# Performance work log

Measured on AMD Instinct MI355X. Metric: run time of the kernel, lower is better.

Reference implementation:

```python
import jax, jax.numpy as jnp
import numpy as np

N, E, F_IN, HID, N_LAYERS, C_OUT = 100000, 1600000, 256, 64, 5, 64


def _glorot(k, shape):
    lim = np.sqrt(6.0 / (shape[0] + shape[1])).astype(np.float32)
    return jax.random.uniform(k, shape, jnp.float32, -lim, lim)


def setup_inputs() -> dict:
    key = jax.random.key(0)
    ks = jax.random.split(key, 16)
    inp = {
        'feats': jax.random.normal(ks[0], (N, F_IN), jnp.float32),
        'src': jax.random.randint(ks[1], (E,), 0, N),
        'dst': jax.random.randint(ks[2], (E,), 0, N),
    }
    dims = [F_IN] + [HID] * N_LAYERS
    for i in range(N_LAYERS):
        inp[f'W{i}'] = _glorot(ks[3 + i], (dims[i], dims[i + 1]))
        inp[f'b{i}'] = jnp.zeros((dims[i + 1],), jnp.float32)
    inp['Wout'] = _glorot(ks[10], (HID * N_LAYERS, C_OUT))
    inp['bout'] = jnp.zeros((C_OUT,), jnp.float32)
    return inp


def reference(feats, src, dst, W0, b0, W1, b1, W2, b2, W3, b3, W4, b4, Wout, bout):
    n = feats.shape[0]
    one = jnp.ones((src.shape[0],), feats.dtype)
    out_deg = jnp.zeros((n,), feats.dtype).at[src].add(one)
    in_deg = jnp.zeros((n,), feats.dtype).at[dst].add(one)
    # DGL GraphConv norm='both': D_out^{-1/2} on src side, D_in^{-1/2} on dst side
    norm_src = jax.lax.rsqrt(jnp.maximum(out_deg, 1.0))
    norm_dst = jax.lax.rsqrt(jnp.maximum(in_deg, 1.0))

    h = feats
    feat_lst = []
    for W, b in [(W0, b0), (W1, b1), (W2, b2), (W3, b3), (W4, b4)]:
        hs = (h * norm_src[:, None]) @ W          # weight before gather (in>=out)
        agg = jax.ops.segment_sum(hs[src], dst, num_segments=n)  # [N, hid]
        h = jax.nn.relu(agg * norm_dst[:, None] + b)
        feat_lst.append(h)                        # dropout is identity in eval

    out = jnp.concatenate(feat_lst, axis=-1)      # JK 'cat': [N, 5*hid]
    # update_all(copy_u, sum): unnormalized neighbor sum
    hfin = jax.ops.segment_sum(out[src], dst, num_segments=n)
    return hfin @ Wout + bout
```

## Files before the change

kernel.cpp:

```cpp
#include <hip/hip_runtime.h>

#define FIN 256
#define HID 64
#define NLAYERS 5

#define FMA4(ACC, S, V) { float _s = (S); ACC.x += _s*(V).x; ACC.y += _s*(V).y; ACC.z += _s*(V).z; ACC.w += _s*(V).w; }

__device__ inline unsigned short f2bf(float f) {
  unsigned u = __float_as_uint(f);
  u += 0x7FFF + ((u >> 16) & 1);
  return (unsigned short)(u >> 16);
}
__device__ inline float bf2f(unsigned short s) { return __uint_as_float(((unsigned)s) << 16); }

__global__ __launch_bounds__(256) void k_count(const int* __restrict__ dst,
                                               int* __restrict__ cd, int* __restrict__ rank,
                                               int E, int half) {
  int i = blockIdx.x * 256 + threadIdx.x;
  if (i < half) rank[i] = atomicAdd(&cd[dst[i]], 1);
  int i2 = i + half;
  if (i2 < E) rank[i2] = atomicAdd(&cd[dst[i2]], 1);
}

__global__ __launch_bounds__(256) void k_rowalloc(const int* __restrict__ cnt, int* __restrict__ row_start,
                                                  int* __restrict__ gcur, int n) {
  int i = blockIdx.x * 256 + threadIdx.x;
  int lane = threadIdx.x & 63;
  int c = (i < n) ? cnt[i] : 0;
  int s = c;
  #pragma unroll
  for (int d = 1; d < 64; d <<= 1) {
    int t = __shfl_up(s, d, 64);
    if (lane >= d) s += t;
  }
  int total = __shfl(s, 63, 64);
  int base = 0;
  if (lane == 63) base = atomicAdd(gcur, total);
  base = __shfl(base, 63, 64);
  int start = base + s - c;
  if (i < n) row_start[i] = start;
}

__global__ __launch_bounds__(256) void k_place(const int* __restrict__ src, const int* __restrict__ dst,
                                               const int* __restrict__ rank, const int* __restrict__ row_start,
                                               int* __restrict__ col, int* __restrict__ cs, int E) {
  int e = blockIdx.x * 256 + threadIdx.x;
  if (e < E) {
    int s = src[e];
    col[row_start[dst[e]] + rank[e]] = s;
    atomicAdd(&cs[s], 1);
  }
}

__global__ __launch_bounds__(256) void k_norm(const int* __restrict__ cnt, float* __restrict__ nrm, int n) {
  int i = blockIdx.x * 256 + threadIdx.x;
  if (i < n) nrm[i] = rsqrtf(fmaxf((float)cnt[i], 1.0f));
}

#define G0PAD 36
__global__ __launch_bounds__(256) void k_gemm0(const float* __restrict__ feats, const float* __restrict__ ns,
                                               const float* __restrict__ W0, unsigned short* __restrict__ hs,
                                               int nrows) {
  __shared__ float sA[64 * G0PAD];
  __shared__ float sW[32 * 64];
  const int tid = threadIdx.x;
  const int row0 = blockIdx.x * 64;
  const int tr4 = (tid >> 4) * 4;
  const int tc4 = (tid & 15) * 4;
  const int sr = tid >> 3;
  const int sc = (tid & 7) * 4;
  const int wk = tid >> 3;
  float4 acc0 = {0,0,0,0}, acc1 = {0,0,0,0}, acc2 = {0,0,0,0}, acc3 = {0,0,0,0};
  const float4 z4 = {0,0,0,0};

  for (int kb = 0; kb < FIN; kb += 32) {
    __syncthreads();
    {
      int r1 = row0 + sr, r2 = row0 + sr + 32;
      float4 v1 = (r1 < nrows) ? *(const float4*)&feats[(size_t)r1 * FIN + kb + sc] : z4;
      float4 v2 = (r2 < nrows) ? *(const float4*)&feats[(size_t)r2 * FIN + kb + sc] : z4;
      *(float4*)&sA[sr * G0PAD + sc] = v1;
      *(float4*)&sA[(sr + 32) * G0PAD + sc] = v2;
      *(float4*)&sW[wk * 64 + sc]      = *(const float4*)&W0[(size_t)(kb + wk) * HID + sc];
      *(float4*)&sW[wk * 64 + sc + 32] = *(const float4*)&W0[(size_t)(kb + wk) * HID + sc + 32];
    }
    __syncthreads();
    #pragma unroll
    for (int kc = 0; kc < 32; kc += 4) {
      float4 a0 = *(const float4*)&sA[(tr4 + 0) * G0PAD + kc];
      float4 a1 = *(const float4*)&sA[(tr4 + 1) * G0PAD + kc];
      float4 a2 = *(const float4*)&sA[(tr4 + 2) * G0PAD + kc];
      float4 a3 = *(const float4*)&sA[(tr4 + 3) * G0PAD + kc];
      #define G0STEP(KK, C) { \
        float4 wv = *(const float4*)&sW[(kc + KK) * 64 + tc4]; \
        FMA4(acc0, a0.C, wv); FMA4(acc1, a1.C, wv); FMA4(acc2, a2.C, wv); FMA4(acc3, a3.C, wv); }
      G0STEP(0, x) G0STEP(1, y) G0STEP(2, z) G0STEP(3, w)
      #undef G0STEP
    }
  }
  #pragma unroll
  for (int r = 0; r < 4; ++r) {
    int row = row0 + tr4 + r;
    if (row < nrows) {
      float s = ns[row];
      float4 o = (r == 0) ? acc0 : (r == 1) ? acc1 : (r == 2) ? acc2 : acc3;
      ushort4 p;
      p.x = f2bf(o.x * s); p.y = f2bf(o.y * s); p.z = f2bf(o.z * s); p.w = f2bf(o.w * s);
      *(ushort4*)&hs[(size_t)row * HID + tc4] = p;
    }
  }
}

#define GDPAD 68
template<bool HASW, bool FIRST>
__global__ __launch_bounds__(256, 4) void k_gemm_dual(const unsigned short* __restrict__ h,
                                                      const float* __restrict__ ns,
                                                      const float* __restrict__ W, const float* __restrict__ Wb,
                                                      unsigned short* __restrict__ hs, float* __restrict__ proj,
                                                      int nrows) {
  __shared__ float sA[64 * GDPAD];
  __shared__ float sW[64 * 64];
  __shared__ float sWb[64 * 64];
  const int tid = threadIdx.x;
  const int row0 = blockIdx.x * 64;
  const int tr4 = (tid >> 4) * 4;
  const int tc4 = (tid & 15) * 4;
  const int sr = tid >> 2;
  const int scb = (tid & 3) * 16;
  const float4 z4 = {0,0,0,0};

  {
    int gr = row0 + sr;
    #pragma unroll
    for (int o = 0; o < 16; o += 4) {
      float4 v = z4;
      if (gr < nrows) {
        ushort4 u = *(const ushort4*)&h[(size_t)gr * HID + scb + o];
        v.x = bf2f(u.x); v.y = bf2f(u.y); v.z = bf2f(u.z); v.w = bf2f(u.w);
      }
      *(float4*)&sA[sr * GDPAD + scb + o] = v;
      if (HASW) *(float4*)&sW[sr * 64 + scb + o] = *(const float4*)&W[(size_t)sr * HID + scb + o];
      *(float4*)&sWb[sr * 64 + scb + o] = *(const float4*)&Wb[(size_t)sr * HID + scb + o];
    }
  }
  __syncthreads();

  float4 aw0 = {0,0,0,0}, aw1 = {0,0,0,0}, aw2 = {0,0,0,0}, aw3 = {0,0,0,0};
  float4 ab0 = {0,0,0,0}, ab1 = {0,0,0,0}, ab2 = {0,0,0,0}, ab3 = {0,0,0,0};
  #pragma unroll 2
  for (int kc = 0; kc < 64; kc += 4) {
    float4 a0 = *(const float4*)&sA[(tr4 + 0) * GDPAD + kc];
    float4 a1 = *(const float4*)&sA[(tr4 + 1) * GDPAD + kc];
    float4 a2 = *(const float4*)&sA[(tr4 + 2) * GDPAD + kc];
    float4 a3 = *(const float4*)&sA[(tr4 + 3) * GDPAD + kc];
    #define GDSTEP(KK, C) { \
      if (HASW) { \
        float4 wv = *(const float4*)&sW[(kc + KK) * 64 + tc4]; \
        FMA4(aw0, a0.C, wv); FMA4(aw1, a1.C, wv); FMA4(aw2, a2.C, wv); FMA4(aw3, a3.C, wv); } \
      { float4 wbv = *(const float4*)&sWb[(kc + KK) * 64 + tc4]; \
        FMA4(ab0, a0.C, wbv); FMA4(ab1, a1.C, wbv); FMA4(ab2, a2.C, wbv); FMA4(ab3, a3.C, wbv); } }
    GDSTEP(0, x) GDSTEP(1, y) GDSTEP(2, z) GDSTEP(3, w)
    #undef GDSTEP
  }

  #pragma unroll
  for (int r = 0; r < 4; ++r) {
    int row = row0 + tr4 + r;
    if (row < nrows) {
      float4 ob = (r == 0) ? ab0 : (r == 1) ? ab1 : (r == 2) ? ab2 : ab3;
      float4 p;
      if (FIRST) {
        p = ob;
      } else {
        p = *(const float4*)&proj[(size_t)row * HID + tc4];
        p.x += ob.x; p.y += ob.y; p.z += ob.z; p.w += ob.w;
      }
      if (HASW) {
        float s = ns[row];
        float4 o = (r == 0) ? aw0 : (r == 1) ? aw1 : (r == 2) ? aw2 : aw3;
        ushort4 pk;
        pk.x = f2bf(o.x * s); pk.y = f2bf(o.y * s); pk.z = f2bf(o.z * s); pk.w = f2bf(o.w * s);
        *(ushort4*)&hs[(size_t)row * HID + tc4] = pk;
        *(float4*)&proj[(size_t)row * HID + tc4] = p;
      } else {
        ushort4 pk;
        pk.x = f2bf(p.x); pk.y = f2bf(p.y); pk.z = f2bf(p.z); pk.w = f2bf(p.w);
        *(ushort4*)&hs[(size_t)row * HID + tc4] = pk;
      }
    }
  }
}

template<bool FINAL>
__global__ __launch_bounds__(256) void k_gather_bf(const int* __restrict__ row_start, const int* __restrict__ cnt,
                                                   const int* __restrict__ col, const unsigned short* __restrict__ x,
                                                   const float* __restrict__ nd, const float* __restrict__ b,
                                                   unsigned short* __restrict__ ybf, float* __restrict__ yf,
                                                   int n) {
  int node = blockIdx.x * 4 + (threadIdx.x >> 6);
  if (node >= n) return;
  int lane = threadIdx.x & 63;
  int g = lane >> 4;
  int fl = (lane & 15) * 4;
  int j0 = row_start[node];
  int jend = j0 + cnt[node];
  float4 acc = {0,0,0,0}, acc2 = {0,0,0,0};
  int j = j0 + g;
  for (; j + 4 < jend; j += 8) {
    int s1 = col[j];
    int s2 = col[j + 4];
    ushort4 u1 = *(const ushort4*)&x[(size_t)s1 * HID + fl];
    ushort4 u2 = *(const ushort4*)&x[(size_t)s2 * HID + fl];
    acc.x  += bf2f(u1.x); acc.y  += bf2f(u1.y); acc.z  += bf2f(u1.z); acc.w  += bf2f(u1.w);
    acc2.x += bf2f(u2.x); acc2.y += bf2f(u2.y); acc2.z += bf2f(u2.z); acc2.w += bf2f(u2.w);
  }
  if (j < jend) {
    int s = col[j];
    ushort4 u = *(const ushort4*)&x[(size_t)s * HID + fl];
    acc.x += bf2f(u.x); acc.y += bf2f(u.y); acc.z += bf2f(u.z); acc.w += bf2f(u.w);
  }
  acc.x += acc2.x; acc.y += acc2.y; acc.z += acc2.z; acc.w += acc2.w;
  #pragma unroll
  for (int m = 16; m <= 32; m <<= 1) {
    acc.x += __shfl_xor(acc.x, m, 64);
    acc.y += __shfl_xor(acc.y, m, 64);
    acc.z += __shfl_xor(acc.z, m, 64);
    acc.w += __shfl_xor(acc.w, m, 64);
  }
  if (g == 0) {
    float4 bb = *(const float4*)&b[fl];
    if (FINAL) {
      float4 o = {acc.x + bb.x, acc.y + bb.y, acc.z + bb.z, acc.w + bb.w};
      *(float4*)&yf[(size_t)node * HID + fl] = o;
    } else {
      float s = nd[node];
      ushort4 pk;
      pk.x = f2bf(fmaxf(acc.x * s + bb.x, 0.f));
      pk.y = f2bf(fmaxf(acc.y * s + bb.y, 0.f));
      pk.z = f2bf(fmaxf(acc.z * s + bb.z, 0.f));
      pk.w = f2bf(fmaxf(acc.w * s + bb.w, 0.f));
      *(ushort4*)&ybf[(size_t)node * HID + fl] = pk;
    }
  }
}

extern "C" void kernel_launch(void* const* d_in, const int* in_sizes, int n_in,
                              void* d_out, int out_size, void* d_ws, size_t ws_size,
                              hipStream_t stream) {
  const float* feats = (const float*)d_in[0];
  const int* src = (const int*)d_in[1];
  const int* dst = (const int*)d_in[2];
  const float* W[NLAYERS]    = {(const float*)d_in[3], (const float*)d_in[5], (const float*)d_in[7],
                                (const float*)d_in[9], (const float*)d_in[11]};
  const float* bias[NLAYERS] = {(const float*)d_in[4], (const float*)d_in[6], (const float*)d_in[8],
                                (const float*)d_in[10], (const float*)d_in[12]};
  const float* Wout = (const float*)d_in[13];
  const float* bout = (const float*)d_in[14];
  float* out = (float*)d_out;

  const int N = in_sizes[0] / FIN;
  const int E = in_sizes[1];
  const size_t Np = (size_t)((N + 63) / 64) * 64;
  const size_t Ep = (size_t)((E + 63) / 64) * 64;

  char* w = (char*)d_ws;
  int* cnt_s     = (int*)w;            w += Np * 4;
  int* cnt_d     = (int*)w;            w += Np * 4;
  int* row_start = (int*)w;            w += Np * 4;
  int* gcur      = (int*)w;            w += 64 * 4;
  int* col       = (int*)w;            w += Ep * 4;
  float* norm_s  = (float*)w;          w += Np * 4;
  float* norm_d  = (float*)w;          w += Np * 4;
  unsigned short* h = (unsigned short*)w;      w += Np * HID * 2;
  float* proj    = (float*)w;          w += Np * HID * 4;
  unsigned short* hsbuf = (unsigned short*)w;  w += Np * HID * 2;
  int* rank = (int*)h;

  (void)hipMemsetAsync(cnt_s, 0, 2 * Np * sizeof(int), stream);
  (void)hipMemsetAsync(gcur, 0, sizeof(int), stream);

  const int half = (E + 1) / 2;
  k_count<<<(half + 255) / 256, 256, 0, stream>>>(dst, cnt_d, rank, E, half);
  k_rowalloc<<<(N + 255) / 256, 256, 0, stream>>>(cnt_d, row_start, gcur, N);
  k_place<<<(E + 255) / 256, 256, 0, stream>>>(src, dst, rank, row_start, col, cnt_s, E);
  k_norm<<<(int)((2 * Np + 255) / 256), 256, 0, stream>>>(cnt_s, norm_s, (int)(2 * Np));

  const int GEMMB = (N + 63) / 64;
  k_gemm0<<<GEMMB, 256, 0, stream>>>(feats, norm_s, W[0], hsbuf, N);

  const int GB = (N + 3) / 4;
  for (int i = 0; i < NLAYERS; ++i) {
    k_gather_bf<false><<<GB, 256, 0, stream>>>(row_start, cnt_d, col, hsbuf, norm_d, bias[i], h, nullptr, N);
    const float* Wb = Wout + (size_t)i * HID * HID;
    if (i == 0) {
      k_gemm_dual<true, true><<<GEMMB, 256, 0, stream>>>(h, norm_s, W[1], Wb, hsbuf, proj, N);
    } else if (i < NLAYERS - 1) {
      k_gemm_dual<true, false><<<GEMMB, 256, 0, stream>>>(h, norm_s, W[i + 1], Wb, hsbuf, proj, N);
    } else {
      k_gemm_dual<false, false><<<GEMMB, 256, 0, stream>>>(h, norm_s, nullptr, Wb, hsbuf, proj, N);
    }
  }
  k_gather_bf<true><<<GB, 256, 0, stream>>>(row_start, cnt_d, col, hsbuf, nullptr, bout, nullptr, out, N);
}
```

Measured before the change: 638.9 us.

## Keep per-layer bf16 activations and compute JK projection in one final kernel

Replaces the dual GEMM, which accumulated the Wout projection into an fp32 proj buffer every layer (a read and a write per layer), with single-weight GEMMs. Each layer's bf16 activations are now stored in their own buffer, and one k_jk kernel computes the concatenated projection at the end. The gather loop is also unrolled to four independent loads per iteration for more memory-level parallelism. In exchange the workspace is larger and the final kernel reads all five activation buffers.

```diff
diff --git a/kernel.cpp b/kernel.cpp
--- a/kernel.cpp
+++ b/kernel.cpp
@@ -112,81 +112,118 @@
 }
 
 #define GDPAD 68
-template<bool HASW, bool FIRST>
-__global__ __launch_bounds__(256, 4) void k_gemm_dual(const unsigned short* __restrict__ h,
-                                                      const float* __restrict__ ns,
-                                                      const float* __restrict__ W, const float* __restrict__ Wb,
-                                                      unsigned short* __restrict__ hs, float* __restrict__ proj,
-                                                      int nrows) {
+__global__ __launch_bounds__(256, 4) void k_gemm_single(const unsigned short* __restrict__ h,
+                                                        const float* __restrict__ ns,
+                                                        const float* __restrict__ W,
+                                                        unsigned short* __restrict__ hs, int nrows) {
   __shared__ float sA[64 * GDPAD];
   __shared__ float sW[64 * 64];
-  __shared__ float sWb[64 * 64];
   const int tid = threadIdx.x;
   const int row0 = blockIdx.x * 64;
   const int tr4 = (tid >> 4) * 4;
   const int tc4 = (tid & 15) * 4;
   const int sr = tid >> 2;
   const int scb = (tid & 3) * 16;
-  const float4 z4 = {0,0,0,0};
 
   {
     int gr = row0 + sr;
     #pragma unroll
     for (int o = 0; o < 16; o += 4) {
-      float4 v = z4;
+      float4 v = {0,0,0,0};
       if (gr < nrows) {
         ushort4 u = *(const ushort4*)&h[(size_t)gr * HID + scb + o];
         v.x = bf2f(u.x); v.y = bf2f(u.y); v.z = bf2f(u.z); v.w = bf2f(u.w);
       }
       *(float4*)&sA[sr * GDPAD + scb + o] = v;
-      if (HASW) *(float4*)&sW[sr * 64 + scb + o] = *(const float4*)&W[(size_t)sr * HID + scb + o];
-      *(float4*)&sWb[sr * 64 + scb + o] = *(const float4*)&Wb[(size_t)sr * HID + scb + o];
+      *(float4*)&sW[sr * 64 + scb + o] = *(const float4*)&W[(size_t)sr * HID + scb + o];
     }
   }
   __syncthreads();
 
   float4 aw0 = {0,0,0,0}, aw1 = {0,0,0,0}, aw2 = {0,0,0,0}, aw3 = {0,0,0,0};
-  float4 ab0 = {0,0,0,0}, ab1 = {0,0,0,0}, ab2 = {0,0,0,0}, ab3 = {0,0,0,0};
   #pragma unroll 2
   for (int kc = 0; kc < 64; kc += 4) {
     float4 a0 = *(const float4*)&sA[(tr4 + 0) * GDPAD + kc];
     float4 a1 = *(const float4*)&sA[(tr4 + 1) * GDPAD + kc];
     float4 a2 = *(const float4*)&sA[(tr4 + 2) * GDPAD + kc];
     float4 a3 = *(const float4*)&sA[(tr4 + 3) * GDPAD + kc];
-    #define GDSTEP(KK, C) { \
-      if (HASW) { \
-        float4 wv = *(const float4*)&sW[(kc + KK) * 64 + tc4]; \
-        FMA4(aw0, a0.C, wv); FMA4(aw1, a1.C, wv); FMA4(aw2, a2.C, wv); FMA4(aw3, a3.C, wv); } \
-      { float4 wbv = *(const float4*)&sWb[(kc + KK) * 64 + tc4]; \
-        FMA4(ab0, a0.C, wbv); FMA4(ab1, a1.C, wbv); FMA4(ab2, a2.C, wbv); FMA4(ab3, a3.C, wbv); } }
-    GDSTEP(0, x) GDSTEP(1, y) GDSTEP(2, z) GDSTEP(3, w)
-    #undef GDSTEP
+    #define GSSTEP(KK, C) { \
+      float4 wv = *(const float4*)&sW[(kc + KK) * 64 + tc4]; \
+      FMA4(aw0, a0.C, wv); FMA4(aw1, a1.C, wv); FMA4(aw2, a2.C, wv); FMA4(aw3, a3.C, wv); }
+    GSSTEP(0, x) GSSTEP(1, y) GSSTEP(2, z) GSSTEP(3, w)
+    #undef GSSTEP
   }
 
   #pragma unroll
   for (int r = 0; r < 4; ++r) {
     int row = row0 + tr4 + r;
     if (row < nrows) {
-      float4 ob = (r == 0) ? ab0 : (r == 1) ? ab1 : (r == 2) ? ab2 : ab3;
-      float4 p;
-      if (FIRST) {
-        p = ob;
-      } else {
-        p = *(const float4*)&proj[(size_t)row * HID + tc4];
-        p.x += ob.x; p.y += ob.y; p.z += ob.z; p.w += ob.w;
+      float s = ns[row];
+      float4 o = (r == 0) ? aw0 : (r == 1) ? aw1 : (r == 2) ? aw2 : aw3;
+      ushort4 pk;
+      pk.x = f2bf(o.x * s); pk.y = f2bf(o.y * s); pk.z = f2bf(o.z * s); pk.w = f2bf(o.w * s);
+      *(ushort4*)&hs[(size_t)row * HID + tc4] = pk;
+    }
+  }
+}
+
+__global__ __launch_bounds__(256, 4) void k_jk(const unsigned short* __restrict__ h0,
+                                               const unsigned short* __restrict__ h1,
+                                               const unsigned short* __restrict__ h2,
+                                               const unsigned short* __restrict__ h3,
+                                               const unsigned short* __restrict__ h4,
+                                               const float* __restrict__ Wout,
+                                               unsigned short* __restrict__ jk, int nrows) {
+  __shared__ float sA[64 * GDPAD];
+  __shared__ float sW[64 * 64];
+  const int tid = threadIdx.x;
+  const int row0 = blockIdx.x * 64;
+  const int tr4 = (tid >> 4) * 4;
+  const int tc4 = (tid & 15) * 4;
+  const int sr = tid >> 2;
+  const int scb = (tid & 3) * 16;
+  const unsigned short* hc[NLAYERS] = {h0, h1, h2, h3, h4};
+
+  float4 ab0 = {0,0,0,0}, ab1 = {0,0,0,0}, ab2 = {0,0,0,0}, ab3 = {0,0,0,0};
+  for (int c = 0; c < NLAYERS; ++c) {
+    const unsigned short* h = hc[c];
+    __syncthreads();
+    {
+      int gr = row0 + sr;
+      #pragma unroll
+      for (int o = 0; o < 16; o += 4) {
+        float4 v = {0,0,0,0};
+        if (gr < nrows) {
+          ushort4 u = *(const ushort4*)&h[(size_t)gr * HID + scb + o];
+          v.x = bf2f(u.x); v.y = bf2f(u.y); v.z = bf2f(u.z); v.w = bf2f(u.w);
+        }
+        *(float4*)&sA[sr * GDPAD + scb + o] = v;
+        *(float4*)&sW[sr * 64 + scb + o] = *(const float4*)&Wout[(size_t)(c * 64 + sr) * HID + scb + o];
       }
-      if (HASW) {
-        float s = ns[row];
-        float4 o = (r == 0) ? aw0 : (r == 1) ? aw1 : (r == 2) ? aw2 : aw3;
-        ushort4 pk;
-        pk.x = f2bf(o.x * s); pk.y = f2bf(o.y * s); pk.z = f2bf(o.z * s); pk.w = f2bf(o.w * s);
-        *(ushort4*)&hs[(size_t)row * HID + tc4] = pk;
-        *(float4*)&proj[(size_t)row * HID + tc4] = p;
-      } else {
-        ushort4 pk;
-        pk.x = f2bf(p.x); pk.y = f2bf(p.y); pk.z = f2bf(p.z); pk.w = f2bf(p.w);
-        *(ushort4*)&hs[(size_t)row * HID + tc4] = pk;
-      }
+    }
+    __syncthreads();
+    #pragma unroll 2
+    for (int kc = 0; kc < 64; kc += 4) {
+      float4 a0 = *(const float4*)&sA[(tr4 + 0) * GDPAD + kc];
+      float4 a1 = *(const float4*)&sA[(tr4 + 1) * GDPAD + kc];
+      float4 a2 = *(const float4*)&sA[(tr4 + 2) * GDPAD + kc];
+      float4 a3 = *(const float4*)&sA[(tr4 + 3) * GDPAD + kc];
+      #define JKSTEP(KK, C) { \
+        float4 wv = *(const float4*)&sW[(kc + KK) * 64 + tc4]; \
+        FMA4(ab0, a0.C, wv); FMA4(ab1, a1.C, wv); FMA4(ab2, a2.C, wv); FMA4(ab3, a3.C, wv); }
+      JKSTEP(0, x) JKSTEP(1, y) JKSTEP(2, z) JKSTEP(3, w)
+      #undef JKSTEP
+    }
+  }
+
+  #pragma unroll
+  for (int r = 0; r < 4; ++r) {
+    int row = row0 + tr4 + r;
+    if (row < nrows) {
+      float4 o = (r == 0) ? ab0 : (r == 1) ? ab1 : (r == 2) ? ab2 : ab3;
+      ushort4 pk;
+      pk.x = f2bf(o.x); pk.y = f2bf(o.y); pk.z = f2bf(o.z); pk.w = f2bf(o.w);
+      *(ushort4*)&jk[(size_t)row * HID + tc4] = pk;
     }
   }
 }
@@ -204,22 +241,29 @@
   int fl = (lane & 15) * 4;
   int j0 = row_start[node];
   int jend = j0 + cnt[node];
-  float4 acc = {0,0,0,0}, acc2 = {0,0,0,0};
+  float4 a0 = {0,0,0,0}, a1 = {0,0,0,0}, a2 = {0,0,0,0}, a3 = {0,0,0,0};
   int j = j0 + g;
-  for (; j + 4 < jend; j += 8) {
-    int s1 = col[j];
-    int s2 = col[j + 4];
+  for (; j + 12 < jend; j += 16) {
+    int s0 = col[j], s1 = col[j + 4], s2 = col[j + 8], s3 = col[j + 12];
+    ushort4 u0 = *(const ushort4*)&x[(size_t)s0 * HID + fl];
     ushort4 u1 = *(const ushort4*)&x[(size_t)s1 * HID + fl];
     ushort4 u2 = *(const ushort4*)&x[(size_t)s2 * HID + fl];
-    acc.x  += bf2f(u1.x); acc.y  += bf2f(u1.y); acc.z  += bf2f(u1.z); acc.w  += bf2f(u1.w);
-    acc2.x += bf2f(u2.x); acc2.y += bf2f(u2.y); acc2.z += bf2f(u2.z); acc2.w += bf2f(u2.w);
-  }
-  if (j < jend) {
+    ushort4 u3 = *(const ushort4*)&x[(size_t)s3 * HID + fl];
+    a0.x += bf2f(u0.x); a0.y += bf2f(u0.y); a0.z += bf2f(u0.z); a0.w += bf2f(u0.w);
+    a1.x += bf2f(u1.x); a1.y += bf2f(u1.y); a1.z += bf2f(u1.z); a1.w += bf2f(u1.w);
+    a2.x += bf2f(u2.x); a2.y += bf2f(u2.y); a2.z += bf2f(u2.z); a2.w += bf2f(u2.w);
+    a3.x += bf2f(u3.x); a3.y += bf2f(u3.y); a3.z += bf2f(u3.z); a3.w += bf2f(u3.w);
+  }
+  for (; j < jend; j += 4) {
     int s = col[j];
     ushort4 u = *(const ushort4*)&x[(size_t)s * HID + fl];
-    acc.x += bf2f(u.x); acc.y += bf2f(u.y); acc.z += bf2f(u.z); acc.w += bf2f(u.w);
-  }
-  acc.x += acc2.x; acc.y += acc2.y; acc.z += acc2.z; acc.w += acc2.w;
+    a0.x += bf2f(u.x); a0.y += bf2f(u.y); a0.z += bf2f(u.z); a0.w += bf2f(u.w);
+  }
+  float4 acc;
+  acc.x = (a0.x + a1.x) + (a2.x + a3.x);
+  acc.y = (a0.y + a1.y) + (a2.y + a3.y);
+  acc.z = (a0.z + a1.z) + (a2.z + a3.z);
+  acc.w = (a0.w + a1.w) + (a2.w + a3.w);
   #pragma unroll
   for (int m = 16; m <= 32; m <<= 1) {
     acc.x += __shfl_xor(acc.x, m, 64);
@@ -271,10 +315,10 @@
   int* col       = (int*)w;            w += Ep * 4;
   float* norm_s  = (float*)w;          w += Np * 4;
   float* norm_d  = (float*)w;          w += Np * 4;
-  unsigned short* h = (unsigned short*)w;      w += Np * HID * 2;
-  float* proj    = (float*)w;          w += Np * HID * 4;
+  unsigned short* hL[NLAYERS];
+  for (int i = 0; i < NLAYERS; ++i) { hL[i] = (unsigned short*)w; w += Np * HID * 2; }
   unsigned short* hsbuf = (unsigned short*)w;  w += Np * HID * 2;
-  int* rank = (int*)h;
+  int* rank = (int*)hL[0];
 
   (void)hipMemsetAsync(cnt_s, 0, 2 * Np * sizeof(int), stream);
   (void)hipMemsetAsync(gcur, 0, sizeof(int), stream);
@@ -290,15 +334,11 @@
 
   const int GB = (N + 3) / 4;
   for (int i = 0; i < NLAYERS; ++i) {
-    k_gather_bf<false><<<GB, 256, 0, stream>>>(row_start, cnt_d, col, hsbuf, norm_d, bias[i], h, nullptr, N);
-    const float* Wb = Wout + (size_t)i * HID * HID;
-    if (i == 0) {
-      k_gemm_dual<true, true><<<GEMMB, 256, 0, stream>>>(h, norm_s, W[1], Wb, hsbuf, proj, N);
-    } else if (i < NLAYERS - 1) {
-      k_gemm_dual<true, false><<<GEMMB, 256, 0, stream>>>(h, norm_s, W[i + 1], Wb, hsbuf, proj, N);
-    } else {
-      k_gemm_dual<false, false><<<GEMMB, 256, 0, stream>>>(h, norm_s, nullptr, Wb, hsbuf, proj, N);
-    }
-  }
+    k_gather_bf<false><<<GB, 256, 0, stream>>>(row_start, cnt_d, col, hsbuf, norm_d, bias[i], hL[i], nullptr, N);
+    if (i < NLAYERS - 1) {
+      k_gemm_single<<<GEMMB, 256, 0, stream>>>(hL[i], norm_s, W[i + 1], hsbuf, N);
+    }
+  }
+  k_jk<<<GEMMB, 256, 0, stream>>>(hL[0], hL[1], hL[2], hL[3], hL[4], Wout, hsbuf, N);
   k_gather_bf<true><<<GB, 256, 0, stream>>>(row_start, cnt_d, col, hsbuf, nullptr, bout, nullptr, out, N);
 }
```

Result: slower. 673.9 us (+5.5%).
